# Kernel optimization log

Hardware: AMD Instinct MI355X
Metric: run time of the kernel (lower is better)

Reference implementation:

```python
import jax, jax.numpy as jnp
import numpy as np

N_POINTS = 64
N_COLS = 500000
N_ANGS = N_POINTS * (N_POINTS - 1) // 2  # 2016


def setup_inputs() -> dict:
    key = jax.random.key(0)
    k1, k2 = jax.random.split(key)
    X = jax.random.normal(k1, (N_POINTS, N_COLS), dtype=jnp.float32)
    angles = 0.1 * jax.random.normal(k2, (N_ANGS,), dtype=jnp.float32)
    mus = jnp.ones((N_POINTS,), dtype=jnp.float32)
    return {"X": X, "angles": angles, "mus": mus}


def reference(X, angles, mus):
    # X: [n, m]; apply n(n-1)/2 sequential Givens rotations over row pairs
    # in order (iTop, iBtm) for iTop < iBtm, then scale rows by mus.
    # Original torch math per pair: vt' = c*vt - s*vb ; vb' = s*vt + c*vb.
    n = X.shape[0]
    top_np, btm_np = np.triu_indices(n, k=1)  # row-major order matches the double loop
    top = jnp.asarray(top_np, dtype=jnp.int32)
    btm = jnp.asarray(btm_np, dtype=jnp.int32)

    def step(Y, inp):
        a, it, ib = inp
        c = jnp.cos(a)
        s = jnp.sin(a)
        vt = Y[it]  # [m]
        vb = Y[ib]  # [m]
        Y = Y.at[it].set(c * vt - s * vb)
        Y = Y.at[ib].set(s * vt + c * vb)
        return Y, None

    Y, _ = jax.lax.scan(step, X, (angles, top, btm))
    return Y * mus[:, None]
```

## Files before the change

kernel.cpp:

```cpp
#include <hip/hip_runtime.h>
#include <hip/hip_bf16.h>

#define NPTS  64
#define NCOLS 500000
#define NANG  2016

typedef __attribute__((ext_vector_type(8))) short bf16x8;
typedef __attribute__((ext_vector_type(4))) float f32x4;

static __device__ inline short f2bf(float f) {
    union { float f; unsigned u; } uf; uf.f = f;
    unsigned u = uf.u;
    unsigned r = (u + 0x7fffu + ((u >> 16) & 1u)) >> 16;
    return (short)r;
}

__global__ __launch_bounds__(64) void build_M(const float* __restrict__ angles,
                                              const float* __restrict__ mus,
                                              float* __restrict__ Mout) {
    __shared__ float cs[NANG];
    __shared__ float sn[NANG];
    const int tid = threadIdx.x;

    for (int k = tid; k < NANG; k += 64) {
        float a = angles[k];
        cs[k] = cosf(a);
        sn[k] = sinf(a);
    }
    __syncthreads();

    float q[NPTS];
#pragma unroll
    for (int j = 0; j < NPTS; ++j) q[j] = (j == tid) ? 1.0f : 0.0f;

    int k = 0;
#pragma unroll
    for (int i = 0; i < NPTS - 1; ++i) {
#pragma unroll
        for (int ib = i + 1; ib < NPTS; ++ib, ++k) {
            float c = cs[k], s = sn[k];
            float t = q[i];
            float b = q[ib];
            q[ib] = s * t + c * b;
            q[i]  = c * t - s * b;
        }
    }

#pragma unroll
    for (int row = 0; row < NPTS; ++row)
        Mout[row * NPTS + tid] = mus[row] * q[row];
}

__global__ __launch_bounds__(256) void apply_M(const float* __restrict__ X,
                                               const float* __restrict__ M,
                                               float* __restrict__ out,
                                               int nfull, int wstride) {
    const int lane  = threadIdx.x & 63;
    const int wave  = threadIdx.x >> 6;
    const int laneN = lane & 15;
    const int quad  = lane >> 4;

    bf16x8 afrag[4][2];
#pragma unroll
    for (int t = 0; t < 4; ++t) {
#pragma unroll
        for (int q = 0; q < 2; ++q) {
            const float* src = M + (t * 16 + laneN) * NPTS + q * 32 + quad * 8;
            bf16x8 f;
#pragma unroll
            for (int j = 0; j < 8; ++j) f[j] = f2bf(src[j]);
            afrag[t][q] = f;
        }
    }

    const int gw = blockIdx.x * 4 + wave;

    for (int s = gw; s < nfull; s += wstride) {
        const long col0 = (long)s * 64 + 4 * laneN;
        const float* xb = X + col0;

        bf16x8 bfrag[4][2];
#pragma unroll
        for (int q = 0; q < 2; ++q) {
#pragma unroll
            for (int j = 0; j < 8; ++j) {
                const int kk = q * 32 + quad * 8 + j;
                f32x4 v = *(const f32x4*)(xb + (long)kk * NCOLS);
#pragma unroll
                for (int u = 0; u < 4; ++u)
                    bfrag[u][q][j] = f2bf(v[u]);
            }
        }

#pragma unroll
        for (int t = 0; t < 4; ++t) {
            f32x4 acc[4];
#pragma unroll
            for (int u = 0; u < 4; ++u) {
                f32x4 a = {0.f, 0.f, 0.f, 0.f};
                a = __builtin_amdgcn_mfma_f32_16x16x32_bf16(afrag[t][0], bfrag[u][0], a, 0, 0, 0);
                a = __builtin_amdgcn_mfma_f32_16x16x32_bf16(afrag[t][1], bfrag[u][1], a, 0, 0, 0);
                acc[u] = a;
            }
#pragma unroll
            for (int rr = 0; rr < 4; ++rr) {
                const int row = t * 16 + quad * 4 + rr;
                f32x4 o = { acc[0][rr], acc[1][rr], acc[2][rr], acc[3][rr] };
                *(f32x4*)(out + (long)row * NCOLS + col0) = o;
            }
        }
    }

    if (gw < 2) {
        const int col = nfull * 64 + gw * 16 + laneN;
        const float* xb = X + col;
        bf16x8 bfrag[2];
#pragma unroll
        for (int q = 0; q < 2; ++q) {
            bf16x8 f;
#pragma unroll
            for (int j = 0; j < 8; ++j)
                f[j] = f2bf(xb[(long)(q * 32 + quad * 8 + j) * NCOLS]);
            bfrag[q] = f;
        }
#pragma unroll
        for (int t = 0; t < 4; ++t) {
            f32x4 a = {0.f, 0.f, 0.f, 0.f};
            a = __builtin_amdgcn_mfma_f32_16x16x32_bf16(afrag[t][0], bfrag[0], a, 0, 0, 0);
            a = __builtin_amdgcn_mfma_f32_16x16x32_bf16(afrag[t][1], bfrag[1], a, 0, 0, 0);
#pragma unroll
            for (int rr = 0; rr < 4; ++rr)
                out[(long)(t * 16 + quad * 4 + rr) * NCOLS + col] = a[rr];
        }
    }
}

extern "C" void kernel_launch(void* const* d_in, const int* in_sizes, int n_in,
                              void* d_out, int out_size, void* d_ws, size_t ws_size,
                              hipStream_t stream) {
    const float* X      = (const float*)d_in[0];
    const float* angles = (const float*)d_in[1];
    const float* mus    = (const float*)d_in[2];
    float* out = (float*)d_out;
    float* M   = (float*)d_ws;

    build_M<<<1, 64, 0, stream>>>(angles, mus, M);

    const int nfull  = NCOLS / 64;
    const int blocks = 1024;
    apply_M<<<blocks, 256, 0, stream>>>(X, M, out, nfull, blocks * 4);
}
```

Before: 322.3 us.

## Restructure build_M with shared-memory Q, add nontemporal stores, retune grid

```diff
diff --git a/kernel.cpp b/kernel.cpp
--- a/kernel.cpp
+++ b/kernel.cpp
@@ -18,37 +18,62 @@
 __global__ __launch_bounds__(64) void build_M(const float* __restrict__ angles,
                                               const float* __restrict__ mus,
                                               float* __restrict__ Mout) {
-    __shared__ float cs[NANG];
-    __shared__ float sn[NANG];
+    __shared__ float  Q[NPTS][NPTS + 1];
+    __shared__ float2 CSN[NANG];
     const int tid = threadIdx.x;
 
     for (int k = tid; k < NANG; k += 64) {
         float a = angles[k];
-        cs[k] = cosf(a);
-        sn[k] = sinf(a);
+        float s, c;
+        sincosf(a, &s, &c);
+        CSN[k] = make_float2(c, s);
     }
+#pragma unroll
+    for (int r0 = 0; r0 < NPTS; ++r0)
+        Q[r0][tid] = (r0 == tid) ? 1.0f : 0.0f;
     __syncthreads();
 
-    float q[NPTS];
+    int k = 0;
+    float r = Q[0][tid];
+    for (int i = 0; i < NPTS - 1; ++i) {
+        int ib = i + 1;
+        const int n = (NPTS - 1) - i;
+        float  bb[8];
+        float2 cs0[8];
+        int cur = n < 8 ? n : 8;
 #pragma unroll
-    for (int j = 0; j < NPTS; ++j) q[j] = (j == tid) ? 1.0f : 0.0f;
-
-    int k = 0;
+        for (int j = 0; j < 8; ++j)
+            if (j < cur) { bb[j] = Q[ib + j][tid]; cs0[j] = CSN[k + j]; }
+        int done = 0;
+        while (done < n) {
+            int nxt = n - done - cur;
+            if (nxt > 8) nxt = 8;
+            float  b2[8];
+            float2 cs2[8];
 #pragma unroll
-    for (int i = 0; i < NPTS - 1; ++i) {
+            for (int j = 0; j < 8; ++j)
+                if (j < nxt) { b2[j] = Q[ib + cur + j][tid]; cs2[j] = CSN[k + cur + j]; }
 #pragma unroll
-        for (int ib = i + 1; ib < NPTS; ++ib, ++k) {
-            float c = cs[k], s = sn[k];
-            float t = q[i];
-            float b = q[ib];
-            q[ib] = s * t + c * b;
-            q[i]  = c * t - s * b;
+            for (int j = 0; j < 8; ++j)
+                if (j < cur) {
+                    float c = cs0[j].x, s = cs0[j].y, b = bb[j];
+                    Q[ib + j][tid] = s * r + c * b;
+                    r = c * r - s * b;
+                }
+            ib += cur; k += cur; done += cur;
+            cur = nxt;
+#pragma unroll
+            for (int j = 0; j < 8; ++j) { bb[j] = b2[j]; cs0[j] = cs2[j]; }
         }
+        Q[i][tid] = r;
+        r = Q[i + 1][tid];
     }
+    Q[NPTS - 1][tid] = r;
+    __syncthreads();
 
 #pragma unroll
     for (int row = 0; row < NPTS; ++row)
-        Mout[row * NPTS + tid] = mus[row] * q[row];
+        Mout[row * NPTS + tid] = mus[row] * Q[row][tid];
 }
 
 __global__ __launch_bounds__(256) void apply_M(const float* __restrict__ X,
@@ -106,7 +131,7 @@
             for (int rr = 0; rr < 4; ++rr) {
                 const int row = t * 16 + quad * 4 + rr;
                 f32x4 o = { acc[0][rr], acc[1][rr], acc[2][rr], acc[3][rr] };
-                *(f32x4*)(out + (long)row * NCOLS + col0) = o;
+                __builtin_nontemporal_store(o, (f32x4*)(out + (long)row * NCOLS + col0));
             }
         }
     }
@@ -130,7 +155,8 @@
             a = __builtin_amdgcn_mfma_f32_16x16x32_bf16(afrag[t][1], bfrag[1], a, 0, 0, 0);
 #pragma unroll
             for (int rr = 0; rr < 4; ++rr)
-                out[(long)(t * 16 + quad * 4 + rr) * NCOLS + col] = a[rr];
+                __builtin_nontemporal_store(a[rr],
+                    out + (long)(t * 16 + quad * 4 + rr) * NCOLS + col);
         }
     }
 }
@@ -147,6 +173,6 @@
     build_M<<<1, 64, 0, stream>>>(angles, mus, M);
 
     const int nfull  = NCOLS / 64;
-    const int blocks = 1024;
+    const int blocks = 1953;
     apply_M<<<blocks, 256, 0, stream>>>(X, M, out, nfull, blocks * 4);
 }
```

Measured after the change: 377.9 us. 1.17x slower.
